# Kernel tuning notes

Hardware: AMD Instinct MI355X
Metric: run time of the kernel (lower is better)

The kernel has to match this reference:

```python
import jax, jax.numpy as jnp
import numpy as np

NUM_GRAPHS = 512


def setup_inputs() -> dict:
    key = jax.random.key(0)
    ks = jax.random.split(key, 12)
    N, F = 100000, 9
    E = 1600000
    x = jax.random.normal(ks[0], (N, F), dtype=jnp.float32)
    edge_index = jax.random.randint(ks[1], (2, E), 0, N, dtype=jnp.int64)
    batch = jnp.sort(jax.random.randint(ks[2], (N,), 0, NUM_GRAPHS, dtype=jnp.int64))
    def lin(k, fan_in, fan_out):
        k1, k2 = jax.random.split(k)
        bound = 1.0 / np.sqrt(fan_in)
        W = jax.random.uniform(k1, (fan_out, fan_in), jnp.float32, -bound, bound)
        b = jax.random.uniform(k2, (fan_out,), jnp.float32, -bound, bound)
        return W, b
    W1, b1 = lin(ks[3], F, 64)
    W2, b2 = lin(ks[4], 64, 128)
    W3, b3 = lin(ks[5], 128, 64)
    Wfc, bfc = lin(ks[6], 64, 11)
    return {"x": x, "edge_index": edge_index, "batch": batch,
            "W1": W1, "b1": b1, "W2": W2, "b2": b2,
            "W3": W3, "b3": b3, "Wfc": Wfc, "bfc": bfc}


def reference(x, edge_index, batch, W1, b1, W2, b2, W3, b3, Wfc, bfc):
    N = x.shape[0]
    src, dst = edge_index[0], edge_index[1]

    def gin_layer(h, W, b):
        # GINConv (eps=0): Lin((1+eps)*h_i + sum_{j->i} h_j), then relu
        agg = jax.ops.segment_sum(h[src], dst, num_segments=N)
        return jax.nn.relu((h + agg) @ W.T + b)

    h = gin_layer(x, W1, b1)   # [N, 64]
    h = gin_layer(h, W2, b2)   # [N, 128]
    h = gin_layer(h, W3, b3)   # [N, 64]

    # global_mean_pool over graph ids
    sums = jax.ops.segment_sum(h, batch, num_segments=NUM_GRAPHS)           # [G, 64]
    counts = jax.ops.segment_sum(jnp.ones((N,), h.dtype), batch,
                                 num_segments=NUM_GRAPHS)                   # [G]
    pooled = sums / jnp.maximum(counts, 1.0)[:, None]
    return pooled @ Wfc.T + bfc  # [G, num_classes]
```

## Files before the change

### kernel.cpp

```cpp
#include <hip/hip_runtime.h>
#include <hip/hip_bf16.h>


#define NBLK 256
#define CFBS 512
#define RB   128
#define NBMAX 1024
#define SCBS 1024

__device__ inline float bf2f(unsigned short u) {
    return __uint_as_float((unsigned)u << 16);
}
__device__ inline unsigned short f2bf(float f) {
    unsigned x = __float_as_uint(f);
    return (unsigned short)((x + 0x7FFFu + ((x >> 16) & 1u)) >> 16);
}
__device__ inline float lo16(unsigned u) { return __uint_as_float(u << 16); }
__device__ inline float hi16(unsigned u) { return __uint_as_float(u & 0xFFFF0000u); }


__global__ __launch_bounds__(CFBS) void count_kernel(
    const int* __restrict__ dst, int* __restrict__ cnt, int E, int NB)
{
    __shared__ int hist[NBMAX];
    int tid = threadIdx.x;
    for (int i = tid; i < NBMAX; i += CFBS) hist[i] = 0;
    __syncthreads();
    for (int e = blockIdx.x * CFBS + tid; e < E; e += NBLK * CFBS)
        atomicAdd(&hist[dst[e] >> 7], 1);
    __syncthreads();
    for (int b = tid; b < NB; b += CFBS)
        cnt[b * NBLK + blockIdx.x] = hist[b];
}

__global__ __launch_bounds__(SCBS) void scan_k1(
    const int* __restrict__ cnt, int* __restrict__ ofs,
    int* __restrict__ part, int NT)
{
    __shared__ int tmp[SCBS];
    int i = blockIdx.x * SCBS + threadIdx.x;
    int v = (i < NT) ? cnt[i] : 0;
    tmp[threadIdx.x] = v;
    __syncthreads();
    for (int off = 1; off < SCBS; off <<= 1) {
        int t = (threadIdx.x >= off) ? tmp[threadIdx.x - off] : 0;
        __syncthreads();
        tmp[threadIdx.x] += t;
        __syncthreads();
    }
    if (i < NT) ofs[i] = tmp[threadIdx.x] - v;
    if (threadIdx.x == SCBS - 1) part[blockIdx.x] = tmp[threadIdx.x];
}

__global__ __launch_bounds__(SCBS) void scan_k2(int* __restrict__ part, int B)
{
    __shared__ int tmp[SCBS];
    int v = (threadIdx.x < B) ? part[threadIdx.x] : 0;
    tmp[threadIdx.x] = v;
    __syncthreads();
    for (int off = 1; off < SCBS; off <<= 1) {
        int t = (threadIdx.x >= off) ? tmp[threadIdx.x - off] : 0;
        __syncthreads();
        tmp[threadIdx.x] += t;
        __syncthreads();
    }
    if (threadIdx.x < B) part[threadIdx.x] = tmp[threadIdx.x] - v;
}

__global__ __launch_bounds__(SCBS) void scan_k3(
    int* __restrict__ ofs, const int* __restrict__ part, int NT)
{
    int i = blockIdx.x * SCBS + threadIdx.x;
    if (i < NT) ofs[i] += part[blockIdx.x];
}

__global__ __launch_bounds__(CFBS) void fillp_kernel(
    const int* __restrict__ src, const int* __restrict__ dst,
    const int* __restrict__ ofs, int* __restrict__ pairs, int E, int NB)
{
    __shared__ int cur[NBMAX];
    int tid = threadIdx.x;
    for (int b = tid; b < NB; b += CFBS)
        cur[b] = ofs[b * NBLK + blockIdx.x];
    __syncthreads();
    for (int e = blockIdx.x * CFBS + tid; e < E; e += NBLK * CFBS) {
        int d = dst[e];
        int b = d >> 7, dl = d & 127;
        int pos = atomicAdd(&cur[b], 1);
        pairs[pos] = (dl << 20) | src[e];
    }
}

__global__ __launch_bounds__(512) void bucket_csr_kernel(
    const int* __restrict__ pairs, const int* __restrict__ ofs,
    int* __restrict__ rowstart, int* __restrict__ eidx, int N, int E, int NB)
{
    __shared__ int deg[RB], pfx[RB], cur[RB];
    int tid = threadIdx.x;
    int b = blockIdx.x, n0 = b << 7;
    int e0 = ofs[b * NBLK];
    int e1 = (b + 1 < NB) ? ofs[(b + 1) * NBLK] : E;
    if (tid < RB) deg[tid] = 0;
    __syncthreads();
    for (int e = e0 + tid; e < e1; e += 512)
        atomicAdd(&deg[pairs[e] >> 20], 1);
    __syncthreads();
    if (tid < RB) pfx[tid] = deg[tid];
    __syncthreads();
    for (int off = 1; off < RB; off <<= 1) {
        int t = (tid < RB && tid >= off) ? pfx[tid - off] : 0;
        __syncthreads();
        if (tid < RB) pfx[tid] += t;
        __syncthreads();
    }
    if (tid < RB) {
        int ex = pfx[tid] - deg[tid];
        cur[tid] = ex;
        int n = n0 + tid;
        if (n < N) rowstart[n] = e0 + ex;
    }
    if (b == NB - 1 && tid == 0) rowstart[N] = E;
    __syncthreads();
    for (int e = e0 + tid; e < e1; e += 512) {
        int p = pairs[e];
        int pos = e0 + atomicAdd(&cur[p >> 20], 1);
        eidx[pos] = p & 0xFFFFF;
    }
}


__global__ __launch_bounds__(256) void xprep_kernel(
    const float* __restrict__ x, unsigned short* __restrict__ xb, int N)
{
    int n = blockIdx.x * 256 + threadIdx.x;
    if (n >= N) return;
    unsigned short r[16];
    #pragma unroll
    for (int k = 0; k < 9; ++k) r[k] = f2bf(x[(size_t)n * 9 + k]);
    #pragma unroll
    for (int k = 9; k < 16; ++k) r[k] = 0;
    uint4 u0, u1;
    u0.x = r[0] | ((unsigned)r[1] << 16);  u0.y = r[2] | ((unsigned)r[3] << 16);
    u0.z = r[4] | ((unsigned)r[5] << 16);  u0.w = r[6] | ((unsigned)r[7] << 16);
    u1.x = r[8] | ((unsigned)r[9] << 16);  u1.y = 0; u1.z = 0; u1.w = 0;
    *(uint4*)&xb[(size_t)n * 16]     = u0;
    *(uint4*)&xb[(size_t)n * 16 + 8] = u1;
}


__global__ __launch_bounds__(256) void node1v_kernel(
    const unsigned short* __restrict__ xb, const int* __restrict__ rs,
    const int* __restrict__ eidx, const float* __restrict__ W1,
    const float* __restrict__ b1, unsigned short* __restrict__ h1, int N)
{
    __shared__ float Wl[576];
    __shared__ float bl[64];
    for (int i = threadIdx.x; i < 576; i += 256) Wl[i] = W1[i];
    if (threadIdx.x < 64) bl[threadIdx.x] = b1[threadIdx.x];
    __syncthreads();
    int n = blockIdx.x * 4 + (threadIdx.x >> 6);
    if (n >= N) return;
    int lane = threadIdx.x & 63;
    int g  = lane >> 2;
    int d4 = lane & 3;
    float a0 = 0.f, a1 = 0.f, a2 = 0.f, a3 = 0.f;
    if (g == 0) {
        uint2 u = *(const uint2*)&xb[(size_t)n * 16 + d4 * 4];
        a0 += lo16(u.x); a1 += hi16(u.x); a2 += lo16(u.y); a3 += hi16(u.y);
    }
    int e0 = rs[n], e1 = rs[n + 1];
    for (int e = e0; e < e1; e += 16) {
        int idx = e + g;
        if (idx < e1) {
            int s = eidx[idx];
            uint2 u = *(const uint2*)&xb[(size_t)s * 16 + d4 * 4];
            a0 += lo16(u.x); a1 += hi16(u.x); a2 += lo16(u.y); a3 += hi16(u.y);
        }
    }
    #pragma unroll
    for (int m = 4; m < 64; m <<= 1) {
        a0 += __shfl_xor(a0, m); a1 += __shfl_xor(a1, m);
        a2 += __shfl_xor(a2, m); a3 += __shfl_xor(a3, m);
    }
    float xv[9];
    xv[0] = __shfl(a0, 0); xv[1] = __shfl(a1, 0); xv[2] = __shfl(a2, 0);
    xv[3] = __shfl(a3, 0); xv[4] = __shfl(a0, 1); xv[5] = __shfl(a1, 1);
    xv[6] = __shfl(a2, 1); xv[7] = __shfl(a3, 1); xv[8] = __shfl(a0, 2);
    float s = bl[lane];
    const float* wr = &Wl[lane * 9];
    #pragma unroll
    for (int k = 0; k < 9; ++k) s += xv[k] * wr[k];
    h1[(size_t)n * 64 + lane] = f2bf(fmaxf(s, 0.f));
}


template<bool BIAS_RELU, typename OT>
__global__ __launch_bounds__(256) void gather64v_kernel(
    const unsigned short* __restrict__ feat, const int* __restrict__ rs,
    const int* __restrict__ eidx, const float* __restrict__ bias,
    OT* __restrict__ out, int N)
{
    int n = blockIdx.x * 4 + (threadIdx.x >> 6);
    if (n >= N) return;
    int lane = threadIdx.x & 63;
    int g  = lane >> 4;
    int d4 = lane & 15;
    float a0 = 0.f, a1 = 0.f, a2 = 0.f, a3 = 0.f;
    if (g == 0) {
        uint2 u = *(const uint2*)&feat[(size_t)n * 64 + d4 * 4];
        a0 += lo16(u.x); a1 += hi16(u.x); a2 += lo16(u.y); a3 += hi16(u.y);
    }
    int e0 = rs[n], e1 = rs[n + 1];
    int e = e0;
    for (; e + 8 <= e1; e += 8) {
        int sA = eidx[e + g];
        int sB = eidx[e + 4 + g];
        uint2 uA = *(const uint2*)&feat[(size_t)sA * 64 + d4 * 4];
        uint2 uB = *(const uint2*)&feat[(size_t)sB * 64 + d4 * 4];
        a0 += lo16(uA.x); a1 += hi16(uA.x); a2 += lo16(uA.y); a3 += hi16(uA.y);
        a0 += lo16(uB.x); a1 += hi16(uB.x); a2 += lo16(uB.y); a3 += hi16(uB.y);
    }
    for (; e < e1; e += 4) {
        int idx = e + g;
        if (idx < e1) {
            int s = eidx[idx];
            uint2 u = *(const uint2*)&feat[(size_t)s * 64 + d4 * 4];
            a0 += lo16(u.x); a1 += hi16(u.x); a2 += lo16(u.y); a3 += hi16(u.y);
        }
    }
    a0 += __shfl_xor(a0, 16); a1 += __shfl_xor(a1, 16);
    a2 += __shfl_xor(a2, 16); a3 += __shfl_xor(a3, 16);
    a0 += __shfl_xor(a0, 32); a1 += __shfl_xor(a1, 32);
    a2 += __shfl_xor(a2, 32); a3 += __shfl_xor(a3, 32);
    if (g == 0) {
        if (BIAS_RELU) {
            float4 bv = *(const float4*)&bias[d4 * 4];
            a0 = fmaxf(a0 + bv.x, 0.f); a1 = fmaxf(a1 + bv.y, 0.f);
            a2 = fmaxf(a2 + bv.z, 0.f); a3 = fmaxf(a3 + bv.w, 0.f);
        }
        if constexpr (sizeof(OT) == 4) {
            *(float4*)&out[(size_t)n * 64 + d4 * 4] = make_float4(a0, a1, a2, a3);
        } else {
            ushort4 u;
            u.x = f2bf(a0); u.y = f2bf(a1); u.z = f2bf(a2); u.w = f2bf(a3);
            *(ushort4*)&out[(size_t)n * 64 + d4 * 4] = u;
        }
    }
}


template<int IN, int OUT, bool RELU>
__global__ __launch_bounds__(256) void linear_mfma_kernel(
    const unsigned short* __restrict__ A, const float* __restrict__ W,
    const float* __restrict__ bias, unsigned short* __restrict__ Y, int N)
{
    using s8v = __attribute__((ext_vector_type(8))) short;
    using f4v = __attribute__((ext_vector_type(4))) float;
    constexpr int KT = IN / 32;
    constexpr int CT = OUT / 16;
    constexpr int INP = IN + 8;
    __shared__ __align__(16) unsigned short Wb[OUT * INP];
    __shared__ float bl[OUT];
    int tid = threadIdx.x;
    for (int i = tid; i < OUT * IN; i += 256) {
        int o = i / IN, k = i % IN;
        Wb[o * INP + k] = f2bf(W[i]);
    }
    for (int i = tid; i < OUT; i += 256) bl[i] = bias ? bias[i] : 0.f;
    __syncthreads();

    int w = tid >> 6, lane = tid & 63;
    int n0 = blockIdx.x * 64 + w * 16;
    int hl = lane >> 4;
    int ll = lane & 15;

    int an = n0 + ll;
    if (an >= N) an = N - 1;
    const unsigned short* arow = &A[(size_t)an * IN + hl * 8];
    s8v a[KT];
    #pragma unroll
    for (int ks = 0; ks < KT; ++ks) a[ks] = *(const s8v*)&arow[ks * 32];

    f4v acc[CT];
    #pragma unroll
    for (int c = 0; c < CT; ++c) acc[c] = (f4v){0.f, 0.f, 0.f, 0.f};
    #pragma unroll
    for (int c = 0; c < CT; ++c) {
        const unsigned short* wrow = &Wb[(c * 16 + ll) * INP + hl * 8];
        #pragma unroll
        for (int ks = 0; ks < KT; ++ks) {
            s8v b = *(const s8v*)&wrow[ks * 32];
            acc[c] = __builtin_amdgcn_mfma_f32_16x16x32_bf16(a[ks], b, acc[c], 0, 0, 0);
        }
    }
    #pragma unroll
    for (int c = 0; c < CT; ++c) {
        int col = c * 16 + ll;
        float bv = bl[col];
        #pragma unroll
        for (int r = 0; r < 4; ++r) {
            int gn = n0 + hl * 4 + r;
            if (gn < N) {
                float v = acc[c][r] + bv;
                if (RELU) v = fmaxf(v, 0.f);
                Y[(size_t)gn * OUT + col] = f2bf(v);
            }
        }
    }
}


__device__ inline int lower_bound_i(const int* a, int n, int v) {
    int lo = 0, hi = n;
    while (lo < hi) {
        int mid = (lo + hi) >> 1;
        if (a[mid] < v) lo = mid + 1; else hi = mid;
    }
    return lo;
}

__global__ __launch_bounds__(256) void pool_fc_kernel(
    const unsigned short* __restrict__ h3, const int* __restrict__ batch,
    const float* __restrict__ Wfc, const float* __restrict__ bfc,
    float* __restrict__ out, int N)
{
    int g = blockIdx.x;
    int tid = threadIdx.x;
    int w = tid >> 6, lane = tid & 63;
    int lo = lower_bound_i(batch, N, g);
    int hi = lower_bound_i(batch, N, g + 1);
    float sum = 0.f;
    for (int i = lo + w; i < hi; i += 4)
        sum += bf2f(h3[(size_t)i * 64 + lane]);
    __shared__ float P[4][64];
    P[w][lane] = sum;
    __syncthreads();
    if (w == 0) {
        float s = P[0][lane] + P[1][lane] + P[2][lane] + P[3][lane];
        float cnt = (float)((hi - lo) > 0 ? (hi - lo) : 1);
        P[0][lane] = s / cnt;
    }
    __syncthreads();
    if (tid < 11) {
        float s = bfc[tid];
        const float* wr = &Wfc[tid * 64];
        #pragma unroll 8
        for (int k = 0; k < 64; ++k) s += P[0][k] * wr[k];
        out[g * 11 + tid] = s;
    }
}


extern "C" void kernel_launch(void* const* d_in, const int* in_sizes, int n_in,
                              void* d_out, int out_size, void* d_ws, size_t ws_size,
                              hipStream_t stream) {
    const float* x    = (const float*)d_in[0];
    const int*   ei   = (const int*)d_in[1];
    const int*   batch= (const int*)d_in[2];
    const float* W1   = (const float*)d_in[3];
    const float* b1   = (const float*)d_in[4];
    const float* W2   = (const float*)d_in[5];
    const float* b2   = (const float*)d_in[6];
    const float* W3   = (const float*)d_in[7];
    const float* b3   = (const float*)d_in[8];
    const float* Wfc  = (const float*)d_in[9];
    const float* bfc  = (const float*)d_in[10];
    float* out = (float*)d_out;

    const int N = in_sizes[2];
    const int E = in_sizes[1] / 2;
    const int G = out_size / 11;
    const int* src = ei;
    const int* dst = ei + E;
    const int NB = (N + RB - 1) / RB;
    const int NT = NB * NBLK;
    const int SB = (NT + SCBS - 1) / SCBS;

    unsigned short* B1 = (unsigned short*)d_ws;
    unsigned short* B2 = B1 + (size_t)64 * N;
    unsigned short* B3 = B2 + (size_t)64 * N;
    unsigned short* XB = B3 + (size_t)128 * N;
    int* pairs    = (int*)(XB + (size_t)16 * N);
    int* eidx     = pairs + E;
    int* rowstart = eidx + E;
    int* cnt      = rowstart + (N + 1);
    int* ofs      = cnt + NT;
    int* part     = ofs + NT;

    unsigned short* h1   = B1;
    unsigned short* buf2 = B2;
    unsigned short* h2   = B3;
    unsigned short* t3   = B1;
    unsigned short* h3   = B2;
    unsigned short* xb   = XB;

    count_kernel<<<NBLK, CFBS, 0, stream>>>(dst, cnt, E, NB);
    scan_k1<<<SB, SCBS, 0, stream>>>(cnt, ofs, part, NT);
    scan_k2<<<1, SCBS, 0, stream>>>(part, SB);
    scan_k3<<<SB, SCBS, 0, stream>>>(ofs, part, NT);
    fillp_kernel<<<NBLK, CFBS, 0, stream>>>(src, dst, ofs, pairs, E, NB);
    bucket_csr_kernel<<<NB, 512, 0, stream>>>(pairs, ofs, rowstart, eidx, N, E, NB);
    xprep_kernel<<<(N + 255) / 256, 256, 0, stream>>>(x, xb, N);

    node1v_kernel<<<(N + 3) / 4, 256, 0, stream>>>(
        xb, rowstart, eidx, W1, b1, h1, N);

    gather64v_kernel<false, unsigned short><<<(N + 3) / 4, 256, 0, stream>>>(
        h1, rowstart, eidx, nullptr, buf2, N);
    linear_mfma_kernel<64, 128, true><<<(N + 63) / 64, 256, 0, stream>>>(
        buf2, W2, b2, h2, N);

    linear_mfma_kernel<128, 64, false><<<(N + 63) / 64, 256, 0, stream>>>(
        h2, W3, nullptr, t3, N);
    gather64v_kernel<true, unsigned short><<<(N + 3) / 4, 256, 0, stream>>>(
        t3, rowstart, eidx, b3, h3, N);

    pool_fc_kernel<<<G, 256, 0, stream>>>(h3, batch, Wfc, bfc, out, N);
}
```

Baseline: 241.6 us.

## Process four nodes per wavefront in gather kernels with shuffled edge indices

The first-layer aggregation kernel and both 64-wide gather kernels now give each wavefront four destination nodes instead of one, and launch four times fewer blocks. Edge indices are loaded coalesced, 64 at a time per node, and broadcast with shuffles. Feature loads for the four nodes are interleaved so more independent memory requests are in flight. The cost is masked extra loads up to the largest degree among the four nodes, plus higher register use for the four sets of accumulators.

```diff
diff --git a/kernel.cpp b/kernel.cpp
--- a/kernel.cpp
+++ b/kernel.cpp
@@ -158,92 +158,153 @@
     for (int i = threadIdx.x; i < 576; i += 256) Wl[i] = W1[i];
     if (threadIdx.x < 64) bl[threadIdx.x] = b1[threadIdx.x];
     __syncthreads();
-    int n = blockIdx.x * 4 + (threadIdx.x >> 6);
-    if (n >= N) return;
+    int wid = threadIdx.x >> 6;
     int lane = threadIdx.x & 63;
     int g  = lane >> 2;
     int d4 = lane & 3;
-    float a0 = 0.f, a1 = 0.f, a2 = 0.f, a3 = 0.f;
-    if (g == 0) {
-        uint2 u = *(const uint2*)&xb[(size_t)n * 16 + d4 * 4];
-        a0 += lo16(u.x); a1 += hi16(u.x); a2 += lo16(u.y); a3 += hi16(u.y);
-    }
-    int e0 = rs[n], e1 = rs[n + 1];
-    for (int e = e0; e < e1; e += 16) {
-        int idx = e + g;
-        if (idx < e1) {
-            int s = eidx[idx];
-            uint2 u = *(const uint2*)&xb[(size_t)s * 16 + d4 * 4];
-            a0 += lo16(u.x); a1 += hi16(u.x); a2 += lo16(u.y); a3 += hi16(u.y);
+    int nb = blockIdx.x * 16 + wid * 4;
+    if (nb >= N) return;
+
+    int n[4], e0[4], dg[4];
+    float A0[4], A1[4], A2[4], A3[4];
+    #pragma unroll
+    for (int i = 0; i < 4; ++i) {
+        n[i] = min(nb + i, N - 1);
+        e0[i] = rs[n[i]];
+        dg[i] = rs[n[i] + 1] - e0[i];
+        A0[i] = A1[i] = A2[i] = A3[i] = 0.f;
+    }
+    #pragma unroll
+    for (int i = 0; i < 4; ++i) {
+        if (g == 0) {
+            uint2 u = *(const uint2*)&xb[(size_t)n[i] * 16 + d4 * 4];
+            A0[i] += lo16(u.x); A1[i] += hi16(u.x);
+            A2[i] += lo16(u.y); A3[i] += hi16(u.y);
+        }
+    }
+    int mdeg = max(max(dg[0], dg[1]), max(dg[2], dg[3]));
+    for (int w0 = 0; w0 < mdeg; w0 += 64) {
+        int sidx[4], wd[4];
+        #pragma unroll
+        for (int i = 0; i < 4; ++i) {
+            wd[i] = min(max(dg[i] - w0, 0), 64);
+            sidx[i] = (lane < wd[i]) ? eidx[e0[i] + w0 + lane] : 0;
+        }
+        int mwd = max(max(wd[0], wd[1]), max(wd[2], wd[3]));
+        for (int c = 0; c < mwd; c += 16) {
+            #pragma unroll
+            for (int i = 0; i < 4; ++i) {
+                int idx = c + g;
+                int s = __shfl(sidx[i], idx < wd[i] ? idx : 0);
+                float m = (idx < wd[i]) ? 1.f : 0.f;
+                uint2 u = *(const uint2*)&xb[(size_t)s * 16 + d4 * 4];
+                A0[i] += m * lo16(u.x); A1[i] += m * hi16(u.x);
+                A2[i] += m * lo16(u.y); A3[i] += m * hi16(u.y);
+            }
         }
     }
     #pragma unroll
     for (int m = 4; m < 64; m <<= 1) {
-        a0 += __shfl_xor(a0, m); a1 += __shfl_xor(a1, m);
-        a2 += __shfl_xor(a2, m); a3 += __shfl_xor(a3, m);
-    }
-    float xv[9];
-    xv[0] = __shfl(a0, 0); xv[1] = __shfl(a1, 0); xv[2] = __shfl(a2, 0);
-    xv[3] = __shfl(a3, 0); xv[4] = __shfl(a0, 1); xv[5] = __shfl(a1, 1);
-    xv[6] = __shfl(a2, 1); xv[7] = __shfl(a3, 1); xv[8] = __shfl(a0, 2);
-    float s = bl[lane];
+        #pragma unroll
+        for (int i = 0; i < 4; ++i) {
+            A0[i] += __shfl_xor(A0[i], m); A1[i] += __shfl_xor(A1[i], m);
+            A2[i] += __shfl_xor(A2[i], m); A3[i] += __shfl_xor(A3[i], m);
+        }
+    }
     const float* wr = &Wl[lane * 9];
     #pragma unroll
-    for (int k = 0; k < 9; ++k) s += xv[k] * wr[k];
-    h1[(size_t)n * 64 + lane] = f2bf(fmaxf(s, 0.f));
-}
-
-
-template<bool BIAS_RELU, typename OT>
+    for (int i = 0; i < 4; ++i) {
+        float xv0 = __shfl(A0[i], 0), xv1 = __shfl(A1[i], 0);
+        float xv2 = __shfl(A2[i], 0), xv3 = __shfl(A3[i], 0);
+        float xv4 = __shfl(A0[i], 1), xv5 = __shfl(A1[i], 1);
+        float xv6 = __shfl(A2[i], 1), xv7 = __shfl(A3[i], 1);
+        float xv8 = __shfl(A0[i], 2);
+        float s = bl[lane] + xv0 * wr[0] + xv1 * wr[1] + xv2 * wr[2]
+                + xv3 * wr[3] + xv4 * wr[4] + xv5 * wr[5] + xv6 * wr[6]
+                + xv7 * wr[7] + xv8 * wr[8];
+        if (nb + i < N)
+            h1[(size_t)(nb + i) * 64 + lane] = f2bf(fmaxf(s, 0.f));
+    }
+}
+
+
+template<bool BIAS_RELU>
 __global__ __launch_bounds__(256) void gather64v_kernel(
     const unsigned short* __restrict__ feat, const int* __restrict__ rs,
     const int* __restrict__ eidx, const float* __restrict__ bias,
-    OT* __restrict__ out, int N)
-{
-    int n = blockIdx.x * 4 + (threadIdx.x >> 6);
-    if (n >= N) return;
+    unsigned short* __restrict__ out, int N)
+{
+    int wid = threadIdx.x >> 6;
     int lane = threadIdx.x & 63;
     int g  = lane >> 4;
     int d4 = lane & 15;
-    float a0 = 0.f, a1 = 0.f, a2 = 0.f, a3 = 0.f;
-    if (g == 0) {
-        uint2 u = *(const uint2*)&feat[(size_t)n * 64 + d4 * 4];
-        a0 += lo16(u.x); a1 += hi16(u.x); a2 += lo16(u.y); a3 += hi16(u.y);
-    }
-    int e0 = rs[n], e1 = rs[n + 1];
-    int e = e0;
-    for (; e + 8 <= e1; e += 8) {
-        int sA = eidx[e + g];
-        int sB = eidx[e + 4 + g];
-        uint2 uA = *(const uint2*)&feat[(size_t)sA * 64 + d4 * 4];
-        uint2 uB = *(const uint2*)&feat[(size_t)sB * 64 + d4 * 4];
-        a0 += lo16(uA.x); a1 += hi16(uA.x); a2 += lo16(uA.y); a3 += hi16(uA.y);
-        a0 += lo16(uB.x); a1 += hi16(uB.x); a2 += lo16(uB.y); a3 += hi16(uB.y);
-    }
-    for (; e < e1; e += 4) {
-        int idx = e + g;
-        if (idx < e1) {
-            int s = eidx[idx];
-            uint2 u = *(const uint2*)&feat[(size_t)s * 64 + d4 * 4];
-            a0 += lo16(u.x); a1 += hi16(u.x); a2 += lo16(u.y); a3 += hi16(u.y);
-        }
-    }
-    a0 += __shfl_xor(a0, 16); a1 += __shfl_xor(a1, 16);
-    a2 += __shfl_xor(a2, 16); a3 += __shfl_xor(a3, 16);
-    a0 += __shfl_xor(a0, 32); a1 += __shfl_xor(a1, 32);
-    a2 += __shfl_xor(a2, 32); a3 += __shfl_xor(a3, 32);
-    if (g == 0) {
-        if (BIAS_RELU) {
-            float4 bv = *(const float4*)&bias[d4 * 4];
-            a0 = fmaxf(a0 + bv.x, 0.f); a1 = fmaxf(a1 + bv.y, 0.f);
-            a2 = fmaxf(a2 + bv.z, 0.f); a3 = fmaxf(a3 + bv.w, 0.f);
-        }
-        if constexpr (sizeof(OT) == 4) {
-            *(float4*)&out[(size_t)n * 64 + d4 * 4] = make_float4(a0, a1, a2, a3);
-        } else {
+    int nb = blockIdx.x * 16 + wid * 4;
+    if (nb >= N) return;
+
+    int n[4], e0[4], dg[4];
+    float A0[4], A1[4], A2[4], A3[4];
+    #pragma unroll
+    for (int i = 0; i < 4; ++i) {
+        n[i] = min(nb + i, N - 1);
+        e0[i] = rs[n[i]];
+        dg[i] = rs[n[i] + 1] - e0[i];
+        A0[i] = A1[i] = A2[i] = A3[i] = 0.f;
+    }
+    #pragma unroll
+    for (int i = 0; i < 4; ++i) {
+        if (g == 0) {
+            uint2 u = *(const uint2*)&feat[(size_t)n[i] * 64 + d4 * 4];
+            A0[i] += lo16(u.x); A1[i] += hi16(u.x);
+            A2[i] += lo16(u.y); A3[i] += hi16(u.y);
+        }
+    }
+    int mdeg = max(max(dg[0], dg[1]), max(dg[2], dg[3]));
+    for (int w0 = 0; w0 < mdeg; w0 += 64) {
+        int sidx[4], wd[4];
+        #pragma unroll
+        for (int i = 0; i < 4; ++i) {
+            wd[i] = min(max(dg[i] - w0, 0), 64);
+            sidx[i] = (lane < wd[i]) ? eidx[e0[i] + w0 + lane] : 0;
+        }
+        int mwd = max(max(wd[0], wd[1]), max(wd[2], wd[3]));
+        for (int c = 0; c < mwd; c += 8) {
+            #pragma unroll
+            for (int i = 0; i < 4; ++i) {
+                int i0 = c + g, i1 = c + 4 + g;
+                int s0 = __shfl(sidx[i], i0 < wd[i] ? i0 : 0);
+                int s1 = __shfl(sidx[i], i1 < wd[i] ? i1 : 0);
+                float m0 = (i0 < wd[i]) ? 1.f : 0.f;
+                float m1 = (i1 < wd[i]) ? 1.f : 0.f;
+                uint2 u0 = *(const uint2*)&feat[(size_t)s0 * 64 + d4 * 4];
+                uint2 u1 = *(const uint2*)&feat[(size_t)s1 * 64 + d4 * 4];
+                A0[i] += m0 * lo16(u0.x) + m1 * lo16(u1.x);
+                A1[i] += m0 * hi16(u0.x) + m1 * hi16(u1.x);
+                A2[i] += m0 * lo16(u0.y) + m1 * lo16(u1.y);
+                A3[i] += m0 * hi16(u0.y) + m1 * hi16(u1.y);
+            }
+        }
+    }
+    #pragma unroll
+    for (int m = 16; m < 64; m <<= 1) {
+        #pragma unroll
+        for (int i = 0; i < 4; ++i) {
+            A0[i] += __shfl_xor(A0[i], m); A1[i] += __shfl_xor(A1[i], m);
+            A2[i] += __shfl_xor(A2[i], m); A3[i] += __shfl_xor(A3[i], m);
+        }
+    }
+    float4 bv = make_float4(0.f, 0.f, 0.f, 0.f);
+    if (BIAS_RELU) bv = *(const float4*)&bias[d4 * 4];
+    #pragma unroll
+    for (int i = 0; i < 4; ++i) {
+        if (g == 0 && nb + i < N) {
+            float a0 = A0[i], a1 = A1[i], a2 = A2[i], a3 = A3[i];
+            if (BIAS_RELU) {
+                a0 = fmaxf(a0 + bv.x, 0.f); a1 = fmaxf(a1 + bv.y, 0.f);
+                a2 = fmaxf(a2 + bv.z, 0.f); a3 = fmaxf(a3 + bv.w, 0.f);
+            }
             ushort4 u;
             u.x = f2bf(a0); u.y = f2bf(a1); u.z = f2bf(a2); u.w = f2bf(a3);
-            *(ushort4*)&out[(size_t)n * 64 + d4 * 4] = u;
+            *(ushort4*)&out[(size_t)(nb + i) * 64 + d4 * 4] = u;
         }
     }
 }
@@ -402,17 +463,17 @@
     bucket_csr_kernel<<<NB, 512, 0, stream>>>(pairs, ofs, rowstart, eidx, N, E, NB);
     xprep_kernel<<<(N + 255) / 256, 256, 0, stream>>>(x, xb, N);
 
-    node1v_kernel<<<(N + 3) / 4, 256, 0, stream>>>(
+    node1v_kernel<<<(N + 15) / 16, 256, 0, stream>>>(
         xb, rowstart, eidx, W1, b1, h1, N);
 
-    gather64v_kernel<false, unsigned short><<<(N + 3) / 4, 256, 0, stream>>>(
+    gather64v_kernel<false><<<(N + 15) / 16, 256, 0, stream>>>(
         h1, rowstart, eidx, nullptr, buf2, N);
     linear_mfma_kernel<64, 128, true><<<(N + 63) / 64, 256, 0, stream>>>(
         buf2, W2, b2, h2, N);
 
     linear_mfma_kernel<128, 64, false><<<(N + 63) / 64, 256, 0, stream>>>(
         h2, W3, nullptr, t3, N);
-    gather64v_kernel<true, unsigned short><<<(N + 3) / 4, 256, 0, stream>>>(
+    gather64v_kernel<true><<<(N + 15) / 16, 256, 0, stream>>>(
         t3, rowstart, eidx, b3, h3, N);
 
     pool_fc_kernel<<<G, 256, 0, stream>>>(h3, batch, Wfc, bfc, out, N);
```

Result: faster. 209.6 us (-13.2%).
